# Performance work log

Measured on AMD Instinct MI355X. Metric: run time of the kernel, lower is better.

The kernel has to match this reference:

```python
import jax, jax.numpy as jnp
import numpy as np
import math

B, S, D, H = 2, 1024, 4096, 32
HD = D // H          # head_dim = 128
P = 10               # prompt_len
THETA = 500000.0     # rope_theta


def _rope(t, cos, sin):
    # t: [b, s, h, hd]; pairs (2i, 2i+1) form complex numbers as in view_as_complex
    tr = t[..., 0::2]
    ti = t[..., 1::2]
    c = cos[None, :, None, :]
    s = sin[None, :, None, :]
    out = jnp.stack([tr * c - ti * s, tr * s + ti * c], axis=-1)  # [b,s,h,hd/2,2]
    return out.reshape(t.shape)


def setup_inputs() -> dict:
    key = jax.random.key(0)
    ks = jax.random.split(key, 8)
    sc = 0.02
    x = jax.random.normal(ks[0], (B, S, D), jnp.float32)
    wq = jax.random.normal(ks[1], (D, D), jnp.float32) * sc
    wk = jax.random.normal(ks[2], (D, D), jnp.float32) * sc
    wv = jax.random.normal(ks[3], (D, D), jnp.float32) * sc
    wo = jax.random.normal(ks[4], (D, D), jnp.float32) * sc
    prompt = jax.random.normal(ks[5], (P, D), jnp.float32)
    prompt_gate = jax.random.normal(ks[6], (1, H, 1, 1), jnp.float32) * 0.1
    # RoPE tables (real/imag of freqs_cis)
    inv = 1.0 / (THETA ** (jnp.arange(0, HD, 2, dtype=jnp.float32) / HD))  # [HD/2]
    ang = jnp.outer(jnp.arange(S, dtype=jnp.float32), inv)                 # [S, HD/2]
    freqs_cos = jnp.cos(ang)
    freqs_sin = jnp.sin(ang)
    # causal additive mask
    mask = jnp.triu(jnp.full((S, S), -1e9, jnp.float32), 1)[None, None]
    type_weight = jax.random.uniform(ks[7], (B, S, 1), jnp.float32)
    return dict(x=x, wq=wq, wk=wk, wv=wv, wo=wo, prompt=prompt,
                prompt_gate=prompt_gate, freqs_cos=freqs_cos,
                freqs_sin=freqs_sin, mask=mask, type_weight=type_weight,
                start_pos=0)


def reference(x, wq, wk, wv, wo, prompt, prompt_gate, freqs_cos, freqs_sin,
              mask, type_weight, start_pos):
    # training-mode forward: start_pos == 0, keys/values = current tokens
    scale = 1.0 / math.sqrt(HD)
    xq = (x @ wq.T).reshape(B, S, H, HD)
    xk = (x @ wk.T).reshape(B, S, H, HD)
    xv = (x @ wv.T).reshape(B, S, H, HD)
    xq = _rope(xq, freqs_cos, freqs_sin)
    xk = _rope(xk, freqs_cos, freqs_sin)
    q = xq.transpose(0, 2, 1, 3)  # [b,h,s,hd]
    k = xk.transpose(0, 2, 1, 3)
    v = xv.transpose(0, 2, 1, 3)
    scores = jnp.einsum('bhqd,bhkd->bhqk', q, k) * scale + mask
    probs = jax.nn.softmax(scores, axis=-1)
    out = jnp.einsum('bhqk,bhkd->bhqd', probs, v)  # [b,h,s,hd]
    # gated prompt injection (num_experts == 1); type_weight unused, as in source
    pk = (prompt @ wk.T).reshape(P, H, HD)
    pv = (prompt @ wv.T).reshape(P, H, HD)
    p_scores = jnp.einsum('bhqd,phd->bhqp', q, pk) * scale
    p_probs = prompt_gate * jax.nn.softmax(p_scores, axis=-1)
    p_out = jnp.einsum('bhqp,phd->bhqd', p_probs, pv)
    out = (out + p_out).transpose(0, 2, 1, 3).reshape(B, S, D)
    return out @ wo.T
```

## Files before the change

### kernel.cpp

```cpp
#include <hip/hip_runtime.h>
#include <hip/hip_bf16.h>
#include <stdint.h>

typedef __hip_bfloat16 bf16;
typedef __attribute__((ext_vector_type(8))) short short8;
typedef __attribute__((ext_vector_type(4))) float f32x4;

#define SCALE_ 0.08838834764831845f

static __device__ __forceinline__ float bf2f(short u) {
  unsigned int x = ((unsigned int)(unsigned short)u) << 16;
  return __builtin_bit_cast(float, x);
}
static __device__ __forceinline__ short f2bf(float f) {
  __hip_bfloat16 h = __float2bfloat16(f);
  return __builtin_bit_cast(short, h);
}
static __device__ __forceinline__ f32x4 mfma16(short8 a, short8 b, f32x4 c) {
  return __builtin_amdgcn_mfma_f32_16x16x32_bf16(a, b, c, 0, 0, 0);
}
static __device__ __forceinline__ void gl_lds16(const bf16* g, bf16* l) {
  __builtin_amdgcn_global_load_lds(
      (const __attribute__((address_space(1))) unsigned int*)g,
      (__attribute__((address_space(3))) unsigned int*)l, 16, 0, 0);
}

__global__ __launch_bounds__(256) void cvt6(
    const float* __restrict__ sx, const float* __restrict__ sq,
    const float* __restrict__ sk, const float* __restrict__ sv,
    const float* __restrict__ so, const float* __restrict__ sp,
    bf16* __restrict__ dx, bf16* __restrict__ dq, bf16* __restrict__ dk,
    bf16* __restrict__ dv, bf16* __restrict__ d4, bf16* __restrict__ dp)
{
  int b = blockIdx.x;
  const float* s; bf16* d; int off;
  if (b < 4096)       { s = sx; d = dx; off = b; }
  else if (b < 12288) { s = sq; d = dq; off = b - 4096; }
  else if (b < 20480) { s = sk; d = dk; off = b - 12288; }
  else if (b < 28672) { s = sv; d = dv; off = b - 20480; }
  else if (b < 36864) { s = so; d = d4; off = b - 28672; }
  else                { s = sp; d = dp; off = b - 36864; }
  long base = (long)off * 2048 + threadIdx.x * 8;
  f32x4 a = *(const f32x4*)(s + base);
  f32x4 c = *(const f32x4*)(s + base + 4);
  short8 o;
#pragma unroll
  for (int j = 0; j < 4; j++) { o[j] = f2bf(a[j]); o[4 + j] = f2bf(c[j]); }
  *(short8*)(d + base) = o;
}

template <int NKT, bool KSPLIT>
__global__ __launch_bounds__(512, 2) void gemm_bt(
    const bf16* __restrict__ A, const bf16* __restrict__ A2,
    const bf16* __restrict__ B0, const bf16* __restrict__ B1, const bf16* __restrict__ B2w,
    bf16* __restrict__ C0, bf16* __restrict__ C1, bf16* __restrict__ C2,
    bf16* __restrict__ P1, bf16* __restrict__ P2,
    float* __restrict__ CF,
    int M1, int Mtot)
{
  __shared__ char lds[131072];
  const int tid = threadIdx.x, w = tid >> 6, l = tid & 63;
  const int lr = l & 15, lg = l >> 4;
  const int wm = w >> 2, wn = w & 3;
  const int z = blockIdx.z;
  const bf16* Bw = KSPLIT ? B0 : ((z == 0) ? B0 : ((z == 1) ? B1 : B2w));
  bf16* C  = (z == 0) ? C0 : ((z == 1) ? C1 : C2);
  bf16* Cp = (KSPLIT || z == 0) ? (bf16*)0 : ((z == 1) ? P1 : P2);
  float* CFz = CF;
  long koff = 0;
  if (KSPLIT) { koff = (long)z * NKT * 64; CFz = CF + (long)z * M1 * 4096; }

  const int cpx = gridDim.x >> 3, orig = blockIdx.x;
  const int wg = (orig & 7) * cpx + (orig >> 3);
  const long m0 = (long)(wg >> 4) * 256;
  const long n0 = (long)(wg & 15) * 256;

  const int r0 = ((tid >> 3) << 1) | ((tid >> 2) & 1);
  const int c0 = (tid & 3) ^ ((tid >> 3) & 3);
  const bf16 *pa0, *pa1;
  {
    long mx = (long)(Mtot - M1) - 1;
    long g0 = m0 + r0, g1 = m0 + r0 + 128;
    const bf16 *q0, *q1;
    if (g0 < M1) q0 = A + g0 * 4096;
    else { long rr = g0 - M1; if (rr > mx) rr = mx; q0 = A2 + rr * 4096; }
    if (g1 < M1) q1 = A + g1 * 4096;
    else { long rr = g1 - M1; if (rr > mx) rr = mx; q1 = A2 + rr * 4096; }
    pa0 = q0 + c0 * 8 + koff;
    pa1 = q1 + c0 * 8 + koff;
  }
  const bf16* pb0 = Bw + (n0 + r0) * 4096 + c0 * 8 + koff;
  const bf16* pb1 = pb0 + (long)128 * 4096;

  const int ro  = (lr >> 1) * 128 + (((lr & 1) * 4) + (lg ^ ((lr >> 1) & 3))) * 16;
  const int aro = wm * 8192 + ro;
  const int bro = wn * 4096 + ro;

  f32x4 acc[8][4];
#pragma unroll
  for (int i = 0; i < 8; i++)
#pragma unroll
    for (int j = 0; j < 4; j++) acc[i][j] = (f32x4){0.f, 0.f, 0.f, 0.f};

  short8 af[4], bf[4];

#define STGA(S_, KE_)                                                        \
  {                                                                          \
    bf16* d_ = (bf16*)(lds + (S_) * 16384) + tid * 8;                        \
    gl_lds16(pa0 + (KE_), d_);                                               \
    gl_lds16(pa1 + (KE_), d_ + 4096);                                        \
  }
#define STGB(S_, KE_)                                                        \
  {                                                                          \
    bf16* d_ = (bf16*)(lds + (S_) * 16384) + tid * 8;                        \
    gl_lds16(pb0 + (KE_), d_);                                               \
    gl_lds16(pb1 + (KE_), d_ + 4096);                                        \
  }
#define SYNC(VM_)                                                            \
  {                                                                          \
    asm volatile("s_waitcnt vmcnt(" VM_ ")" ::: "memory");                   \
    __builtin_amdgcn_s_barrier();                                            \
    __builtin_amdgcn_sched_barrier(0);                                       \
  }
#define PHASE(PRB_, AU_, BU_, MO_, LB_, STG_)                                \
  {                                                                          \
    STG_                                                                     \
    const char* ab_ = lds + (PRB_) + (AU_) + aro;                            \
    _Pragma("unroll") for (int mi = 0; mi < 4; mi++)                         \
      af[mi] = *(const short8*)(ab_ + ((MO_) + mi) * 1024);                  \
    if (LB_) {                                                               \
      const char* bb_ = lds + (PRB_) + (BU_) + bro;                          \
      _Pragma("unroll") for (int ni = 0; ni < 4; ni++)                       \
        bf[ni] = *(const short8*)(bb_ + ni * 1024);                          \
    }                                                                        \
    asm volatile("s_waitcnt lgkmcnt(0)" ::: "memory");                       \
    __builtin_amdgcn_sched_barrier(0);                                       \
    __builtin_amdgcn_s_setprio(1);                                           \
    _Pragma("unroll") for (int mi = 0; mi < 4; mi++)                         \
      _Pragma("unroll") for (int ni = 0; ni < 4; ni++)                       \
        acc[(MO_) + mi][ni] = mfma16(af[mi], bf[ni], acc[(MO_) + mi][ni]);   \
    __builtin_amdgcn_s_setprio(0);                                           \
  }
#define KT(PRB_, S6_, S7_, S8_, S9_, KE1_, KE2_)                             \
  SYNC("8") PHASE(PRB_, 0, 16384, 0, 1, STGA(S6_, KE1_))                     \
  PHASE(PRB_, 0, 16384, 4, 0, STGB(S7_, KE1_))                               \
  SYNC("8") PHASE(PRB_, 32768, 49152, 0, 1, STGA(S8_, KE2_))                 \
  PHASE(PRB_, 32768, 49152, 4, 0, STGB(S9_, KE2_))

  STGA(0, 0) STGB(1, 0) STGA(2, 32) STGB(3, 32) STGA(4, 64) STGB(5, 64)

  for (int t = 0; t < NKT - 2; t += 2) {
    const int ka = (t + 1) * 64 + 32, kb = (t + 2) * 64;
    const int kc = (t + 2) * 64 + 32, kd = (t + 3) * 64;
    KT(0, 6, 7, 0, 1, ka, kb)
    KT(65536, 2, 3, 4, 5, kc, kd)
  }
  {
    const int kel = (NKT - 1) * 64 + 32;
    SYNC("8") PHASE(0, 0, 16384, 0, 1, STGA(6, kel))
    PHASE(0, 0, 16384, 4, 0, STGB(7, kel))
    SYNC("8") PHASE(0, 32768, 49152, 0, 1, )
    PHASE(0, 32768, 49152, 4, 0, )
  }
  SYNC("4") PHASE(65536, 0, 16384, 0, 1, )
  PHASE(65536, 0, 16384, 4, 0, )
  SYNC("0") PHASE(65536, 32768, 49152, 0, 1, )
  PHASE(65536, 32768, 49152, 4, 0, )

#undef KT
#undef PHASE
#undef SYNC
#undef STGB
#undef STGA

#pragma unroll
  for (int mi = 0; mi < 8; mi++) {
#pragma unroll
    for (int ni = 0; ni < 4; ni++) {
      long col = n0 + wn * 64 + ni * 16 + lr;
      f32x4 v = acc[mi][ni];
#pragma unroll
      for (int j = 0; j < 4; j++) {
        long row = m0 + wm * 128 + mi * 16 + lg * 4 + j;
        if (CFz) {
          CFz[row * 4096 + col] = v[j];
        } else if (row < M1) {
          *(short*)(C + row * 4096 + col) = f2bf(v[j]);
        } else if (Cp != 0 && row < Mtot) {
          *(short*)(Cp + (row - M1) * 4096 + col) = f2bf(v[j]);
        }
      }
    }
  }
}

__global__ __launch_bounds__(512, 2) void gemm_n128(
    const bf16* __restrict__ A, const bf16* __restrict__ Bw,
    float* __restrict__ CF)
{
  __shared__ char lds[98304];
  const int tid = threadIdx.x, w = tid >> 6, l = tid & 63;
  const int lr = l & 15, lg = l >> 4;
  const int wm = w >> 1, wn = w & 1;

  const int cpx = gridDim.x >> 3, orig = blockIdx.x;
  const int wg = (orig & 7) * cpx + (orig >> 3);
  const long m0 = (long)(wg >> 5) * 256;
  const long n0 = (long)(wg & 31) * 128;

  const int r0 = ((tid >> 3) << 1) | ((tid >> 2) & 1);
  const int c0 = (tid & 3) ^ ((tid >> 3) & 3);
  const bf16* pa0 = A + (m0 + r0) * 4096 + c0 * 8;
  const bf16* pa1 = pa0 + (long)128 * 4096;
  const bf16* pb0 = Bw + (n0 + r0) * 4096 + c0 * 8;

  const int ro  = (lr >> 1) * 128 + (((lr & 1) * 4) + (lg ^ ((lr >> 1) & 3))) * 16;
  const int aro = wm * 4096 + ro;
  const int bro = wn * 4096 + ro;

  f32x4 acc[4][4];
#pragma unroll
  for (int i = 0; i < 4; i++)
#pragma unroll
    for (int j = 0; j < 4; j++) acc[i][j] = (f32x4){0.f, 0.f, 0.f, 0.f};

  short8 af[4], bf[4];

#define NSTGA(SB_, KE_)                                                      \
  {                                                                          \
    bf16* d_ = (bf16*)(lds + (SB_)) + tid * 8;                               \
    gl_lds16(pa0 + (KE_), d_);                                               \
    gl_lds16(pa1 + (KE_), d_ + 4096);                                        \
  }
#define NSTGB(SB_, KE_)                                                      \
  {                                                                          \
    bf16* d_ = (bf16*)(lds + (SB_)) + tid * 8;                               \
    gl_lds16(pb0 + (KE_), d_);                                               \
  }
#define NSYNC(VM_)                                                           \
  {                                                                          \
    asm volatile("s_waitcnt vmcnt(" VM_ ")" ::: "memory");                   \
    __builtin_amdgcn_s_barrier();                                            \
    __builtin_amdgcn_sched_barrier(0);                                       \
  }
#define NPH(PRB_, AO_, BO_, STG_)                                            \
  {                                                                          \
    STG_                                                                     \
    const char* ab_ = lds + (PRB_) + (AO_) + aro;                            \
    _Pragma("unroll") for (int mi = 0; mi < 4; mi++)                         \
      af[mi] = *(const short8*)(ab_ + mi * 1024);                            \
    const char* bb_ = lds + (PRB_) + (BO_) + bro;                            \
    _Pragma("unroll") for (int ni = 0; ni < 4; ni++)                         \
      bf[ni] = *(const short8*)(bb_ + ni * 1024);                            \
    asm volatile("s_waitcnt lgkmcnt(0)" ::: "memory");                       \
    __builtin_amdgcn_sched_barrier(0);                                       \
    __builtin_amdgcn_s_setprio(1);                                           \
    _Pragma("unroll") for (int mi = 0; mi < 4; mi++)                         \
      _Pragma("unroll") for (int ni = 0; ni < 4; ni++)                       \
        acc[mi][ni] = mfma16(af[mi], bf[ni], acc[mi][ni]);                   \
    __builtin_amdgcn_s_setprio(0);                                           \
  }

  NSTGA(0, 0)      NSTGB(16384, 0)
  NSTGA(24576, 32) NSTGB(40960, 32)
  NSTGA(49152, 64) NSTGB(65536, 64)

  for (int t = 0; t < 62; t += 2) {
    const int ka = (t + 1) * 64 + 32;
    const int kb = (t + 2) * 64;
    NSYNC("3") NPH(0, 0, 16384,     NSTGA(49152 + 24576, ka) NSTGB(49152 + 40960, ka))
    NSYNC("3") NPH(0, 24576, 40960, NSTGA(0, kb) NSTGB(16384, kb))
    const int kc = (t + 2) * 64 + 32;
    const int kd = (t + 3) * 64;
    NSYNC("3") NPH(49152, 0, 16384,     NSTGA(24576, kc) NSTGB(40960, kc))
    NSYNC("3") NPH(49152, 24576, 40960, NSTGA(49152, kd) NSTGB(49152 + 16384, kd))
  }
  NSYNC("3") NPH(0, 0, 16384,     NSTGA(49152 + 24576, 63 * 64 + 32) NSTGB(49152 + 40960, 63 * 64 + 32))
  NSYNC("3") NPH(0, 24576, 40960, )
  NSYNC("3") NPH(49152, 0, 16384, )
  NSYNC("0") NPH(49152, 24576, 40960, )

#undef NPH
#undef NSYNC
#undef NSTGB
#undef NSTGA

#pragma unroll
  for (int mi = 0; mi < 4; mi++) {
#pragma unroll
    for (int ni = 0; ni < 4; ni++) {
      long col = n0 + wn * 64 + ni * 16 + lr;
      f32x4 v = acc[mi][ni];
#pragma unroll
      for (int j = 0; j < 4; j++) {
        long row = m0 + wm * 64 + mi * 16 + lg * 4 + j;
        CF[row * 4096 + col] = v[j];
      }
    }
  }
}

__global__ __launch_bounds__(256) void prep_qkv(
    bf16* __restrict__ Q, bf16* __restrict__ Kb,
    const float* __restrict__ FC, const float* __restrict__ FS,
    const bf16* __restrict__ V, bf16* __restrict__ VT)
{
  const int t = threadIdx.x;
  if (blockIdx.y < 2) {
    const int row = blockIdx.x;
    const int s = row & 1023;
    bf16* base = (blockIdx.y ? Kb : Q) + (long)row * 4096 + t * 16;
    short8 v0 = *(const short8*)base;
    short8 v1 = *(const short8*)(base + 8);
    const float* cp = FC + s * 64 + (t & 7) * 8;
    const float* sp = FS + s * 64 + (t & 7) * 8;
    f32x4 c0 = *(const f32x4*)cp;
    f32x4 c1 = *(const f32x4*)(cp + 4);
    f32x4 s0 = *(const f32x4*)sp;
    f32x4 s1 = *(const f32x4*)(sp + 4);
    short8 o0, o1;
#pragma unroll
    for (int j = 0; j < 4; j++) {
      float c = c0[j], sn = s0[j];
      float e = bf2f(v0[2 * j]), od = bf2f(v0[2 * j + 1]);
      o0[2 * j] = f2bf(e * c - od * sn);
      o0[2 * j + 1] = f2bf(e * sn + od * c);
      float c2 = c1[j], sn2 = s1[j];
      float e2 = bf2f(v1[2 * j]), od2 = bf2f(v1[2 * j + 1]);
      o1[2 * j] = f2bf(e2 * c2 - od2 * sn2);
      o1[2 * j + 1] = f2bf(e2 * sn2 + od2 * c2);
    }
    *(short8*)base = o0;
    *(short8*)(base + 8) = o1;
    return;
  }
  if (blockIdx.x >= 1024) return;
  __shared__ bf16 T[64 * 128];
  const int st = (blockIdx.x & 15) * 64, bh = blockIdx.x >> 4;
  const int b = bh >> 5, h = bh & 31;
  const bf16* src = V + ((long)(b * 1024 + st)) * 4096 + h * 128;
#pragma unroll
  for (int rr = 0; rr < 4; ++rr) {
    int i = t + rr * 256;
    int s_l = i >> 4, c = i & 15;
    short8 v = *(const short8*)(src + (long)s_l * 4096 + c * 8);
    *(short8*)((char*)T + s_l * 256 + ((c ^ (s_l & 7)) * 16)) = v;
  }
  __syncthreads();
#pragma unroll
  for (int rr = 0; rr < 4; ++rr) {
    int i = t + rr * 256;
    int d = i >> 3, cs = i & 7;
    short8 ov;
#pragma unroll
    for (int e = 0; e < 8; e++) {
      int s_l = cs * 8 + e;
      ov[e] = *(const short*)((char*)T + s_l * 256 + (((d >> 3) ^ (s_l & 7)) * 16) + (d & 7) * 2);
    }
    *(short8*)(VT + ((long)bh * 128 + d) * 1024 + st + cs * 8) = ov;
  }
}

__global__ __launch_bounds__(256) void flash_attn(
    const bf16* __restrict__ Q, const bf16* __restrict__ Kg, const bf16* __restrict__ VT,
    const bf16* __restrict__ PK, const bf16* __restrict__ PV,
    const float* __restrict__ GATE, bf16* __restrict__ O)
{
  __shared__ bf16 Kl[32 * 128];
  __shared__ bf16 Vl[128 * 32];
  __shared__ bf16 PKl[16 * 128];
  __shared__ bf16 PVl[128 * 16];
  __shared__ bf16 Pl[4][16 * 32];
  const int tid = threadIdx.x, w = tid >> 6, l = tid & 63;
  const int lg = l >> 4, lr = l & 15;
  const int qb = blockIdx.x, bh = blockIdx.y;
  const int b = bh >> 5, h = bh & 31;
  const int q0 = qb * 64 + w * 16;

  short8 qf[4];
  {
    const bf16* qp = Q + ((long)(b * 1024 + q0 + lr)) * 4096 + h * 128 + lg * 8;
#pragma unroll
    for (int c = 0; c < 4; c++) qf[c] = *(const short8*)(qp + c * 32);
  }
  {
    int rowp = tid >> 4, pc = tid & 15, lc = pc ^ (rowp & 7);
    short8 v = {0, 0, 0, 0, 0, 0, 0, 0};
    if (rowp < 10) v = *(const short8*)(PK + (long)rowp * 4096 + h * 128 + lc * 8);
    *(short8*)((char*)PKl + tid * 16) = v;
  }
  {
    int d = tid >> 1, pb = (tid & 1) * 8;
#pragma unroll
    for (int e = 0; e < 8; e++) {
      int p = pb + e;
      short v = 0;
      if (p < 10) v = __builtin_bit_cast(short, PV[(long)p * 4096 + h * 128 + d]);
      *(short*)((char*)PVl + d * 32 + (((p >> 3) ^ (d & 1)) * 16) + (p & 7) * 2) = v;
    }
  }
  const float gate = GATE[h];

  f32x4 o[8];
#pragma unroll
  for (int i = 0; i < 8; i++) o[i] = (f32x4){0.f, 0.f, 0.f, 0.f};
  float m_[4] = {-1e30f, -1e30f, -1e30f, -1e30f};
  float l_[4] = {0.f, 0.f, 0.f, 0.f};

  const int nt = (qb + 1) * 2;
  const bf16* Kbase = Kg + ((long)b * 1024) * 4096 + h * 128;
  const bf16* Vbase = VT + ((long)bh) * 128 * 1024;
  const int cb1 = w * 64, cb2 = 256 + w * 64;
  const int iA = cb1 + l, iB = cb2 + l;
  bf16* pw = &Pl[w][0];

  for (int j = 0; j < nt; ++j) {
    __syncthreads();
    {
      const bf16* gA = Kbase + (long)(j * 32 + (iA >> 4)) * 4096 + ((iA & 15) ^ ((iA >> 4) & 7)) * 8;
      const bf16* gB = Kbase + (long)(j * 32 + (iB >> 4)) * 4096 + ((iB & 15) ^ ((iB >> 4) & 7)) * 8;
      gl_lds16(gA, Kl + cb1 * 8);
      gl_lds16(gB, Kl + cb2 * 8);
      const bf16* vA = Vbase + (long)(iA >> 2) * 1024 + j * 32 + ((iA & 3) ^ ((iA >> 2) & 3)) * 8;
      const bf16* vB = Vbase + (long)(iB >> 2) * 1024 + j * 32 + ((iB & 3) ^ ((iB >> 2) & 3)) * 8;
      gl_lds16(vA, Vl + cb1 * 8);
      gl_lds16(vB, Vl + cb2 * 8);
    }
    __syncthreads();

    f32x4 s[2];
#pragma unroll
    for (int ns = 0; ns < 2; ns++) {
      f32x4 a = (f32x4){0.f, 0.f, 0.f, 0.f};
      int krow = ns * 16 + lr;
      const char* kp = (const char*)Kl + krow * 256;
      int sw = krow & 7;
#pragma unroll
      for (int c = 0; c < 4; c++) {
        short8 kf = *(const short8*)(kp + (((c * 4 + lg) ^ sw) * 16));
        a = mfma16(qf[c], kf, a);
      }
      int key = j * 32 + krow;
#pragma unroll
      for (int r = 0; r < 4; r++) {
        int qr = q0 + lg * 4 + r;
        s[ns][r] = a[r] * SCALE_ + ((key <= qr) ? 0.0f : -1e30f);
      }
    }
    float mx[4], cor[4], sum[4];
#pragma unroll
    for (int r = 0; r < 4; r++) mx[r] = fmaxf(s[0][r], s[1][r]);
#pragma unroll
    for (int xm = 1; xm < 16; xm <<= 1)
#pragma unroll
      for (int r = 0; r < 4; r++) mx[r] = fmaxf(mx[r], __shfl_xor(mx[r], xm, 64));
#pragma unroll
    for (int r = 0; r < 4; r++) {
      float mn = fmaxf(m_[r], mx[r]);
      cor[r] = __expf(m_[r] - mn);
      m_[r] = mn;
      s[0][r] = __expf(s[0][r] - mn);
      s[1][r] = __expf(s[1][r] - mn);
      sum[r] = s[0][r] + s[1][r];
    }
#pragma unroll
    for (int xm = 1; xm < 16; xm <<= 1)
#pragma unroll
      for (int r = 0; r < 4; r++) sum[r] += __shfl_xor(sum[r], xm, 64);
#pragma unroll
    for (int r = 0; r < 4; r++) l_[r] = l_[r] * cor[r] + sum[r];
#pragma unroll
    for (int df = 0; df < 8; df++)
#pragma unroll
      for (int r = 0; r < 4; r++) o[df][r] *= cor[r];

#pragma unroll
    for (int ns = 0; ns < 2; ns++)
#pragma unroll
      for (int r = 0; r < 4; r++)
        *(short*)((char*)pw + ((lg * 4 + r) * 32 + ns * 16 + lr) * 2) = f2bf(s[ns][r]);
    asm volatile("s_waitcnt lgkmcnt(0)" ::: "memory");
    __builtin_amdgcn_sched_barrier(0);
    short8 pf = *(const short8*)(pw + lr * 32 + lg * 8);

#pragma unroll
    for (int df = 0; df < 8; df++) {
      int d = df * 16 + lr;
      short8 vf = *(const short8*)((const char*)Vl + d * 64 + ((lg ^ (d & 3)) * 16));
      o[df] = mfma16(pf, vf, o[df]);
    }
  }

  f32x4 ps;
  {
    f32x4 a = (f32x4){0.f, 0.f, 0.f, 0.f};
    const char* kp = (const char*)PKl + lr * 256;
    int sw = lr & 7;
#pragma unroll
    for (int c = 0; c < 4; c++) {
      short8 kf = *(const short8*)(kp + (((c * 4 + lg) ^ sw) * 16));
      a = mfma16(qf[c], kf, a);
    }
#pragma unroll
    for (int r = 0; r < 4; r++) ps[r] = (lr < 10) ? a[r] * SCALE_ : -1e30f;
  }
  {
    float pm[4], pss[4];
#pragma unroll
    for (int r = 0; r < 4; r++) pm[r] = ps[r];
#pragma unroll
    for (int xm = 1; xm < 16; xm <<= 1)
#pragma unroll
      for (int r = 0; r < 4; r++) pm[r] = fmaxf(pm[r], __shfl_xor(pm[r], xm, 64));
#pragma unroll
    for (int r = 0; r < 4; r++) { ps[r] = __expf(ps[r] - pm[r]); pss[r] = ps[r]; }
#pragma unroll
    for (int xm = 1; xm < 16; xm <<= 1)
#pragma unroll
      for (int r = 0; r < 4; r++) pss[r] += __shfl_xor(pss[r], xm, 64);
#pragma unroll
    for (int r = 0; r < 4; r++) ps[r] = ps[r] / pss[r];
  }
#pragma unroll
  for (int r = 0; r < 4; r++) {
    *(short*)((char*)pw + ((lg * 4 + r) * 32 + lr) * 2) = f2bf(ps[r]);
    *(short*)((char*)pw + ((lg * 4 + r) * 32 + 16 + lr) * 2) = 0;
  }
  asm volatile("s_waitcnt lgkmcnt(0)" ::: "memory");
  __builtin_amdgcn_sched_barrier(0);
  short8 pf2 = *(const short8*)(pw + lr * 32 + lg * 8);
  f32x4 po[8];
#pragma unroll
  for (int df = 0; df < 8; df++) {
    int d = df * 16 + lr;
    short8 vf = {0, 0, 0, 0, 0, 0, 0, 0};
    if (lg < 2) vf = *(const short8*)((const char*)PVl + d * 32 + ((lg ^ (d & 1)) * 16));
    po[df] = mfma16(pf2, vf, (f32x4){0.f, 0.f, 0.f, 0.f});
  }

  bf16* op = O + ((long)(b * 1024 + q0 + lg * 4)) * 4096 + h * 128 + lr;
#pragma unroll
  for (int df = 0; df < 8; df++)
#pragma unroll
    for (int r = 0; r < 4; r++) {
      float val = o[df][r] / l_[r] + gate * po[df][r];
      *(short*)(op + (long)r * 4096 + df * 16) = f2bf(val);
    }
}

extern "C" void kernel_launch(void* const* d_in, const int* in_sizes, int n_in,
                              void* d_out, int out_size, void* d_ws, size_t ws_size,
                              hipStream_t stream) {
  (void)in_sizes; (void)n_in; (void)out_size; (void)ws_size;
  const float* x      = (const float*)d_in[0];
  const float* wq     = (const float*)d_in[1];
  const float* wk     = (const float*)d_in[2];
  const float* wv     = (const float*)d_in[3];
  const float* wo     = (const float*)d_in[4];
  const float* prompt = (const float*)d_in[5];
  const float* gate   = (const float*)d_in[6];
  const float* fcos   = (const float*)d_in[7];
  const float* fsin   = (const float*)d_in[8];
  float* out = (float*)d_out;
  char* ws = (char*)d_ws;

  size_t o = 0;
  bf16* xb  = (bf16*)(ws + o); o += (size_t)8388608 * 2;
  bf16* wqb = (bf16*)(ws + o); o += (size_t)16777216 * 2;
  bf16* wkb = (bf16*)(ws + o); o += (size_t)16777216 * 2;
  bf16* wvb = (bf16*)(ws + o); o += (size_t)16777216 * 2;
  bf16* wob = (bf16*)(ws + o); o += (size_t)16777216 * 2;
  bf16* pb  = (bf16*)(ws + o); o += (size_t)40960 * 2;
  bf16* q_ws  = (bf16*)(ws + o); o += (size_t)2048 * 4096 * 2;
  bf16* k_ws  = (bf16*)(ws + o); o += (size_t)2048 * 4096 * 2;
  bf16* v_ws  = (bf16*)(ws + o); o += (size_t)2048 * 4096 * 2;
  bf16* vT_ws = (bf16*)(ws + o); o += (size_t)2048 * 4096 * 2;
  bf16* pk_ws = (bf16*)(ws + o); o += (size_t)40960 * 2;
  bf16* pv_ws = (bf16*)(ws + o); o += (size_t)40960 * 2;
  bf16* attn_ws = v_ws;

  cvt6<<<dim3(36884), 256, 0, stream>>>(x, wq, wk, wv, wo, prompt,
                                        xb, wqb, wkb, wvb, wob, pb);
  gemm_bt<64, false><<<dim3(144, 1, 3), 512, 0, stream>>>(
      xb, pb, wqb, wkb, wvb, q_ws, k_ws, v_ws, pk_ws, pv_ws, (float*)0, 2048, 2058);
  prep_qkv<<<dim3(2048, 3), 256, 0, stream>>>(q_ws, k_ws, fcos, fsin, v_ws, vT_ws);
  flash_attn<<<dim3(16, 64), 256, 0, stream>>>(
      q_ws, k_ws, vT_ws, pk_ws, pv_ws, gate, attn_ws);
  gemm_n128<<<dim3(256), 512, 0, stream>>>(attn_ws, wob, out);
}
```

Baseline: 508.3 us.

## Double-buffer K/V tiles and widen flash-attention key tile to 64

The flash attention kernel now loads 64-key K/V tiles into two LDS buffers and prefetches tile j+1 with async global-to-LDS loads while tile j is computed. Partial vmcnt waits and raw s_barrier replace the two __syncthreads per iteration. The wider tile halves the loop trip count and the number of softmax reductions per key. In exchange it uses more LDS per block, which may reduce occupancy, and more causal masking is wasted on the diagonal tile.

After: 482.8 us. 5.0% less time.

```diff
diff --git a/kernel.cpp b/kernel.cpp
--- a/kernel.cpp
+++ b/kernel.cpp
@@ -366,11 +366,11 @@
     const bf16* __restrict__ PK, const bf16* __restrict__ PV,
     const float* __restrict__ GATE, bf16* __restrict__ O)
 {
-  __shared__ bf16 Kl[32 * 128];
-  __shared__ bf16 Vl[128 * 32];
+  __shared__ bf16 Kl[2][64 * 128];
+  __shared__ bf16 Vl[2][128 * 64];
   __shared__ bf16 PKl[16 * 128];
   __shared__ bf16 PVl[128 * 16];
-  __shared__ bf16 Pl[4][16 * 32];
+  __shared__ bf16 Pl[4][16 * 64];
   const int tid = threadIdx.x, w = tid >> 6, l = tid & 63;
   const int lg = l >> 4, lr = l & 15;
   const int qb = blockIdx.x, bh = blockIdx.y;
@@ -407,40 +407,51 @@
   float m_[4] = {-1e30f, -1e30f, -1e30f, -1e30f};
   float l_[4] = {0.f, 0.f, 0.f, 0.f};
 
-  const int nt = (qb + 1) * 2;
+  const int nt = qb + 1;
   const bf16* Kbase = Kg + ((long)b * 1024) * 4096 + h * 128;
   const bf16* Vbase = VT + ((long)bh) * 128 * 1024;
-  const int cb1 = w * 64, cb2 = 256 + w * 64;
-  const int iA = cb1 + l, iB = cb2 + l;
   bf16* pw = &Pl[w][0];
 
+#define FSTG(BUF_, J_)                                                        \
+  {                                                                           \
+    _Pragma("unroll") for (int r_ = 0; r_ < 4; ++r_) {                        \
+      int i_ = tid + 256 * r_;                                                \
+      int kr_ = i_ >> 4, kc_ = (i_ & 15) ^ (kr_ & 7);                         \
+      gl_lds16(Kbase + (long)((J_) * 64 + kr_) * 4096 + kc_ * 8,              \
+               &Kl[BUF_][0] + i_ * 8);                                        \
+      int vd_ = i_ >> 3, vc_ = (i_ & 7) ^ (vd_ & 7);                          \
+      gl_lds16(Vbase + (long)vd_ * 1024 + (J_) * 64 + vc_ * 8,                \
+               &Vl[BUF_][0] + i_ * 8);                                        \
+    }                                                                         \
+  }
+
+  FSTG(0, 0)
   for (int j = 0; j < nt; ++j) {
-    __syncthreads();
-    {
-      const bf16* gA = Kbase + (long)(j * 32 + (iA >> 4)) * 4096 + ((iA & 15) ^ ((iA >> 4) & 7)) * 8;
-      const bf16* gB = Kbase + (long)(j * 32 + (iB >> 4)) * 4096 + ((iB & 15) ^ ((iB >> 4) & 7)) * 8;
-      gl_lds16(gA, Kl + cb1 * 8);
-      gl_lds16(gB, Kl + cb2 * 8);
-      const bf16* vA = Vbase + (long)(iA >> 2) * 1024 + j * 32 + ((iA & 3) ^ ((iA >> 2) & 3)) * 8;
-      const bf16* vB = Vbase + (long)(iB >> 2) * 1024 + j * 32 + ((iB & 3) ^ ((iB >> 2) & 3)) * 8;
-      gl_lds16(vA, Vl + cb1 * 8);
-      gl_lds16(vB, Vl + cb2 * 8);
-    }
-    __syncthreads();
-
-    f32x4 s[2];
-#pragma unroll
-    for (int ns = 0; ns < 2; ns++) {
+    __builtin_amdgcn_s_barrier();
+    if (j + 1 < nt) {
+      FSTG((j + 1) & 1, j + 1)
+      asm volatile("s_waitcnt vmcnt(8)" ::: "memory");
+    } else {
+      asm volatile("s_waitcnt vmcnt(0)" ::: "memory");
+    }
+    __builtin_amdgcn_s_barrier();
+    __builtin_amdgcn_sched_barrier(0);
+
+    const char* kb = (const char*)&Kl[j & 1][0];
+    const char* vb = (const char*)&Vl[j & 1][0];
+
+    f32x4 s[4];
+#pragma unroll
+    for (int ns = 0; ns < 4; ns++) {
       f32x4 a = (f32x4){0.f, 0.f, 0.f, 0.f};
       int krow = ns * 16 + lr;
-      const char* kp = (const char*)Kl + krow * 256;
       int sw = krow & 7;
 #pragma unroll
       for (int c = 0; c < 4; c++) {
-        short8 kf = *(const short8*)(kp + (((c * 4 + lg) ^ sw) * 16));
+        short8 kf = *(const short8*)(kb + krow * 256 + (((c * 4 + lg) ^ sw) * 16));
         a = mfma16(qf[c], kf, a);
       }
-      int key = j * 32 + krow;
+      int key = j * 64 + krow;
 #pragma unroll
       for (int r = 0; r < 4; r++) {
         int qr = q0 + lg * 4 + r;
@@ -449,7 +460,8 @@
     }
     float mx[4], cor[4], sum[4];
 #pragma unroll
-    for (int r = 0; r < 4; r++) mx[r] = fmaxf(s[0][r], s[1][r]);
+    for (int r = 0; r < 4; r++)
+      mx[r] = fmaxf(fmaxf(s[0][r], s[1][r]), fmaxf(s[2][r], s[3][r]));
 #pragma unroll
     for (int xm = 1; xm < 16; xm <<= 1)
 #pragma unroll
@@ -459,10 +471,15 @@
       float mn = fmaxf(m_[r], mx[r]);
       cor[r] = __expf(m_[r] - mn);
       m_[r] = mn;
-      s[0][r] = __expf(s[0][r] - mn);
-      s[1][r] = __expf(s[1][r] - mn);
-      sum[r] = s[0][r] + s[1][r];
-    }
+      sum[r] = 0.f;
+    }
+#pragma unroll
+    for (int ns = 0; ns < 4; ns++)
+#pragma unroll
+      for (int r = 0; r < 4; r++) {
+        s[ns][r] = __expf(s[ns][r] - m_[r]);
+        sum[r] += s[ns][r];
+      }
 #pragma unroll
     for (int xm = 1; xm < 16; xm <<= 1)
 #pragma unroll
@@ -475,21 +492,29 @@
       for (int r = 0; r < 4; r++) o[df][r] *= cor[r];
 
 #pragma unroll
-    for (int ns = 0; ns < 2; ns++)
-#pragma unroll
-      for (int r = 0; r < 4; r++)
-        *(short*)((char*)pw + ((lg * 4 + r) * 32 + ns * 16 + lr) * 2) = f2bf(s[ns][r]);
+    for (int ns = 0; ns < 4; ns++)
+#pragma unroll
+      for (int r = 0; r < 4; r++) {
+        int row = lg * 4 + r;
+        int ch = ns * 2 + (lr >> 3);
+        *(short*)((char*)pw + row * 128 + ((ch ^ (row & 7)) * 16) + (lr & 7) * 2)
+            = f2bf(s[ns][r]);
+      }
     asm volatile("s_waitcnt lgkmcnt(0)" ::: "memory");
     __builtin_amdgcn_sched_barrier(0);
-    short8 pf = *(const short8*)(pw + lr * 32 + lg * 8);
+    short8 pf0 = *(const short8*)((char*)pw + lr * 128 + ((lg ^ (lr & 7)) * 16));
+    short8 pf1 = *(const short8*)((char*)pw + lr * 128 + (((4 + lg) ^ (lr & 7)) * 16));
 
 #pragma unroll
     for (int df = 0; df < 8; df++) {
       int d = df * 16 + lr;
-      short8 vf = *(const short8*)((const char*)Vl + d * 64 + ((lg ^ (d & 3)) * 16));
-      o[df] = mfma16(pf, vf, o[df]);
-    }
-  }
+      short8 vf0 = *(const short8*)(vb + d * 128 + ((lg ^ (d & 7)) * 16));
+      short8 vf1 = *(const short8*)(vb + d * 128 + (((4 + lg) ^ (d & 7)) * 16));
+      o[df] = mfma16(pf0, vf0, o[df]);
+      o[df] = mfma16(pf1, vf1, o[df]);
+    }
+  }
+#undef FSTG
 
   f32x4 ps;
   {
@@ -523,12 +548,15 @@
   }
 #pragma unroll
   for (int r = 0; r < 4; r++) {
-    *(short*)((char*)pw + ((lg * 4 + r) * 32 + lr) * 2) = f2bf(ps[r]);
-    *(short*)((char*)pw + ((lg * 4 + r) * 32 + 16 + lr) * 2) = 0;
+    int row = lg * 4 + r;
+    int ch0 = (lr >> 3);
+    *(short*)((char*)pw + row * 128 + ((ch0 ^ (row & 7)) * 16) + (lr & 7) * 2) = f2bf(ps[r]);
+    int ch1 = 2 + (lr >> 3);
+    *(short*)((char*)pw + row * 128 + ((ch1 ^ (row & 7)) * 16) + (lr & 7) * 2) = 0;
   }
   asm volatile("s_waitcnt lgkmcnt(0)" ::: "memory");
   __builtin_amdgcn_sched_barrier(0);
-  short8 pf2 = *(const short8*)(pw + lr * 32 + lg * 8);
+  short8 pf2 = *(const short8*)((char*)pw + lr * 128 + ((lg ^ (lr & 7)) * 16));
   f32x4 po[8];
 #pragma unroll
   for (int df = 0; df < 8; df++) {
```
